# Kernel optimization log

Measured on AMD Instinct MI355X. Metric: run time of the kernel, lower is better.

Reference implementation:

```python
import jax, jax.numpy as jnp
import numpy as np

H = 16          # num_heads
W = 256         # sliding window size
LN_EPS = 1e-6
ROPE_BASE = 10000.0


def layer_norm(x, g, b):
    m = jnp.mean(x, axis=-1, keepdims=True)
    v = jnp.mean((x - m) ** 2, axis=-1, keepdims=True)
    return (x - m) * jax.lax.rsqrt(v + LN_EPS) * g + b


def rope(x):
    # x: [B, S, H, hd]; rotate-half RoPE
    S, hd = x.shape[1], x.shape[-1]
    inv_freq = 1.0 / (ROPE_BASE ** (jnp.arange(0, hd, 2, dtype=jnp.float32) / hd))
    ang = jnp.arange(S, dtype=jnp.float32)[:, None] * inv_freq[None, :]  # [S, hd/2]
    cos = jnp.concatenate([jnp.cos(ang), jnp.cos(ang)], axis=-1)[None, :, None, :]
    sin = jnp.concatenate([jnp.sin(ang), jnp.sin(ang)], axis=-1)[None, :, None, :]
    x1, x2 = jnp.split(x, 2, axis=-1)
    rot = jnp.concatenate([-x2, x1], axis=-1)
    return x * cos + rot * sin


def setup_inputs() -> dict:
    key = jax.random.key(0)
    ks = jax.random.split(key, 12)
    B, S, D, I = 2, 2048, 1024, 4096
    s = 0.02
    return {
        "hidden_states": jax.random.normal(ks[0], (B, S, D), jnp.float32),
        "wq": jax.random.normal(ks[1], (D, D), jnp.float32) * s,
        "wk": jax.random.normal(ks[2], (D, D), jnp.float32) * s,
        "wv": jax.random.normal(ks[3], (D, D), jnp.float32) * s,
        "wo": jax.random.normal(ks[4], (D, D), jnp.float32) * s,
        "w1": jax.random.normal(ks[5], (D, I), jnp.float32) * s,
        "w2": jax.random.normal(ks[6], (I, D), jnp.float32) * s,
        "w3": jax.random.normal(ks[7], (D, I), jnp.float32) * s,
        "ln1_g": jnp.ones((D,), jnp.float32),
        "ln1_b": jnp.zeros((D,), jnp.float32),
        "ln2_g": jnp.ones((D,), jnp.float32),
        "ln2_b": jnp.zeros((D,), jnp.float32),
    }


def reference(hidden_states, wq, wk, wv, wo, w1, w2, w3, ln1_g, ln1_b, ln2_g, ln2_b):
    B, S, D = hidden_states.shape
    hd = D // H

    # --- attention sub-block ---
    residual = hidden_states
    x = layer_norm(hidden_states, ln1_g, ln1_b)
    q = (x @ wq).reshape(B, S, H, hd)
    k = (x @ wk).reshape(B, S, H, hd)
    v = (x @ wv).reshape(B, S, H, hd)
    q, k = rope(q), rope(k)

    scores = jnp.einsum("bqhd,bkhd->bhqk", q, k) / jnp.sqrt(jnp.float32(hd))
    idx = jnp.arange(S)
    rel = idx[:, None] - idx[None, :]          # i - j
    mask = (rel >= 0) & (rel < W)              # causal sliding window
    scores = jnp.where(mask[None, None], scores, jnp.float32(-1e9))
    attn = jax.nn.softmax(scores, axis=-1)
    ctx = jnp.einsum("bhqk,bkhd->bqhd", attn, v).reshape(B, S, D)
    hidden_states = residual + ctx @ wo

    # --- SwiGLU MLP sub-block ---
    residual = hidden_states
    x = layer_norm(hidden_states, ln2_g, ln2_b)
    mlp = (jax.nn.silu(x @ w1) * (x @ w3)) @ w2
    return residual + mlp
```

## Files before the change

kernel.cpp:

```cpp
#include <hip/hip_runtime.h>
#include <hip/hip_bf16.h>

typedef __bf16 bf16_t;
typedef __bf16 bf16x4 __attribute__((ext_vector_type(4)));
typedef __bf16 bf16x8 __attribute__((ext_vector_type(8)));
typedef float f32x4 __attribute__((ext_vector_type(4)));

#define LN_EPS 1e-6f

__device__ __forceinline__ void gl2lds16(const void* g, void* l) {
    __builtin_amdgcn_global_load_lds(
        (const __attribute__((address_space(1))) void*)g,
        (__attribute__((address_space(3))) void*)l, 16, 0, 0);
}

__device__ __forceinline__ void block_sync() {
    __asm__ __volatile__("" ::: "memory");
    __builtin_amdgcn_s_barrier();
    __asm__ __volatile__("" ::: "memory");
}

__global__ void prep_weights_kernel(const float* __restrict__ wq, const float* __restrict__ wk,
                                    const float* __restrict__ wv, const float* __restrict__ wo,
                                    const float* __restrict__ w1, const float* __restrict__ w3,
                                    const float* __restrict__ w2, bf16_t* __restrict__ wq_t,
                                    bf16_t* __restrict__ wk_t, bf16_t* __restrict__ wv_t,
                                    bf16_t* __restrict__ wo_t, bf16_t* __restrict__ w13_t,
                                    bf16_t* __restrict__ w2_t) {
    __shared__ float tile[32][33];
    int id = blockIdx.x;
    const float* src;
    bf16_t* dst;
    int R, C, mode = 0;
    if (id < 4096) {
        int w = id >> 10;
        id &= 1023;
        src = (w == 0) ? wq : (w == 1) ? wk : (w == 2) ? wv : wo;
        dst = (w == 0) ? wq_t : (w == 1) ? wk_t : (w == 2) ? wv_t : wo_t;
        R = 1024; C = 1024;
    } else if (id < 8192) {
        id -= 4096; src = w1; dst = w13_t; R = 1024; C = 4096; mode = 1;
    } else if (id < 12288) {
        id -= 8192; src = w3; dst = w13_t; R = 1024; C = 4096; mode = 2;
    } else {
        id -= 12288; src = w2; dst = w2_t; R = 4096; C = 1024;
    }
    int tpc = C >> 5;
    int bx = id % tpc, by = id / tpc;
    int r0 = by * 32, c0 = bx * 32;
    int tx = threadIdx.x & 31;
    int ty = threadIdx.x >> 5;
#pragma unroll
    for (int i = 0; i < 4; i++) {
        int r = ty + i * 8;
        tile[r][tx] = src[(size_t)(r0 + r) * C + (c0 + tx)];
    }
    __syncthreads();
#pragma unroll
    for (int i = 0; i < 4; i++) {
        int r = ty + i * 8;
        int rr = c0 + r;
        if (mode) rr = ((rr >> 7) << 8) + (rr & 127) + ((mode == 2) ? 128 : 0);
        dst[(size_t)rr * R + (r0 + tx)] = (bf16_t)tile[tx][r];
    }
}

__global__ void ln_kernel(const float* __restrict__ x, const float* __restrict__ g,
                          const float* __restrict__ bb, bf16_t* __restrict__ out, int D) {
    int row = blockIdx.x;
    int t = threadIdx.x;
    const float4* xr = reinterpret_cast<const float4*>(x + (size_t)row * D);
    float4 v = xr[t];
    float s = v.x + v.y + v.z + v.w;
    __shared__ float sbuf[4];
    __shared__ float sbuf2[4];
    int wave = t >> 6, lane = t & 63;
#pragma unroll
    for (int o = 32; o > 0; o >>= 1) s += __shfl_xor(s, o);
    if (lane == 0) sbuf[wave] = s;
    __syncthreads();
    float mean = (sbuf[0] + sbuf[1] + sbuf[2] + sbuf[3]) / (float)D;
    float d0 = v.x - mean, d1 = v.y - mean, d2 = v.z - mean, d3 = v.w - mean;
    float sq = d0 * d0 + d1 * d1 + d2 * d2 + d3 * d3;
#pragma unroll
    for (int o = 32; o > 0; o >>= 1) sq += __shfl_xor(sq, o);
    if (lane == 0) sbuf2[wave] = sq;
    __syncthreads();
    float var = (sbuf2[0] + sbuf2[1] + sbuf2[2] + sbuf2[3]) / (float)D;
    float inv = rsqrtf(var + LN_EPS);
    float4 gv = reinterpret_cast<const float4*>(g)[t];
    float4 bv = reinterpret_cast<const float4*>(bb)[t];
    bf16_t* o0 = out + (size_t)row * D + t * 4;
    o0[0] = (bf16_t)(d0 * inv * gv.x + bv.x);
    o0[1] = (bf16_t)(d1 * inv * gv.y + bv.y);
    o0[2] = (bf16_t)(d2 * inv * gv.z + bv.z);
    o0[3] = (bf16_t)(d3 * inv * gv.w + bv.w);
}

#define G4_BK 64

template <int EPI>
__launch_bounds__(256, 2) __global__
void gemm4_kernel(const bf16_t* __restrict__ A, const bf16_t* __restrict__ Bt,
                  float* __restrict__ Cf, const float* __restrict__ aux,
                  const bf16_t* __restrict__ auxb, bf16_t* __restrict__ Cb,
                  int M, int N, int K, int lda, int ldb) {
    __shared__ __align__(16) bf16_t As[128 * G4_BK];
    __shared__ __align__(16) bf16_t Bs[128 * G4_BK];
    const int t = threadIdx.x;
    const int wave = t >> 6, lane = t & 63;
    const int lr = lane & 15, quad = lane >> 4;
    const int wm = (wave >> 1) * 64, wn = (wave & 1) * 64;

    const int gx = gridDim.x, gy = gridDim.y;
    const int nwg = gx * gy;
    const int lin = blockIdx.y * gx + blockIdx.x;
    const int qch = nwg >> 3;
    const int sw = (lin & 7) * qch + (lin >> 3);
    const int m0 = (sw / gy) * 128;
    const int n0 = (sw % gy) * 128;
    const int koff = blockIdx.z * K;

    const int srow = t >> 3;
    const int sslot = (t & 7) ^ (srow & 7);
    const bf16_t* agp = A + (size_t)(m0 + srow) * lda + koff + sslot * 8;
    const bf16_t* bgp = Bt + (size_t)(n0 + srow) * ldb + koff + sslot * 8;
    bf16_t* asl = As + t * 8;
    bf16_t* bsl = Bs + t * 8;

    int aoff[4][2], boff[4][2];
#pragma unroll
    for (int f = 0; f < 4; f++)
#pragma unroll
        for (int s = 0; s < 2; s++) {
            int ra = wm + f * 16 + lr;
            int rb = wn + f * 16 + lr;
            aoff[f][s] = ra * G4_BK + (((s * 4 + quad) ^ (ra & 7)) << 3);
            boff[f][s] = rb * G4_BK + (((s * 4 + quad) ^ (rb & 7)) << 3);
        }

    f32x4 acc[4][4];
#pragma unroll
    for (int mi = 0; mi < 4; mi++)
#pragma unroll
        for (int ni = 0; ni < 4; ni++) acc[mi][ni] = 0.f;

    for (int k0 = 0; k0 < K; k0 += G4_BK) {
#pragma unroll
        for (int i = 0; i < 4; i++)
            gl2lds16(agp + k0 + (size_t)(32 * i) * lda, asl + i * 2048);
#pragma unroll
        for (int i = 0; i < 4; i++)
            gl2lds16(bgp + k0 + (size_t)(32 * i) * ldb, bsl + i * 2048);
        __syncthreads();
#pragma unroll
        for (int s = 0; s < 2; s++) {
            bf16x8 af[4], bfv[4];
#pragma unroll
            for (int mi = 0; mi < 4; mi++)
                af[mi] = *reinterpret_cast<const bf16x8*>(&As[aoff[mi][s]]);
#pragma unroll
            for (int ni = 0; ni < 4; ni++)
                bfv[ni] = *reinterpret_cast<const bf16x8*>(&Bs[boff[ni][s]]);
#pragma unroll
            for (int mi = 0; mi < 4; mi++)
#pragma unroll
                for (int ni = 0; ni < 4; ni++)
                    acc[mi][ni] = __builtin_amdgcn_mfma_f32_16x16x32_bf16(af[mi], bfv[ni],
                                                                          acc[mi][ni], 0, 0, 0);
        }
        __syncthreads();
    }

#pragma unroll
    for (int mi = 0; mi < 4; mi++)
#pragma unroll
        for (int ni = 0; ni < 4; ni++)
#pragma unroll
            for (int j = 0; j < 4; j++) {
                int gm = m0 + wm + mi * 16 + quad * 4 + j;
                int gn = n0 + wn + ni * 16 + lr;
                size_t idx = (size_t)gm * N + gn;
                float val = acc[mi][ni][j];
                if constexpr (EPI == 1) {
                    Cf[idx] = val + aux[idx];
                }
            }
}


__device__ __forceinline__ void stage_half(const bf16_t* g, int ld, bf16_t* l,
                                           int wave, int lane) {
#pragma unroll
    for (int i = 0; i < 2; i++) {
        int lidx = (wave * 2 + i) * 64 + lane;
        int row = lidx >> 3;
        int ss = (lidx & 7) ^ (row & 7);
        gl2lds16(g + (size_t)row * ld + ss * 8, l + (wave * 2 + i) * 512);
    }
}

template <int QM, int QN>
__device__ __forceinline__ void quad_mfma(f32x4 (&acc)[2][2][4][2], const bf16x8 (&af)[4][2],
                                          const bf16x8 (&bf)[2][2]) {
#pragma unroll
    for (int fr = 0; fr < 4; fr++)
#pragma unroll
        for (int fc = 0; fc < 2; fc++)
#pragma unroll
            for (int ks = 0; ks < 2; ks++)
                acc[QM][QN][fr][fc] = __builtin_amdgcn_mfma_f32_16x16x32_bf16(
                    af[fr][ks], bf[fc][ks], acc[QM][QN][fr][fc], 0, 0, 0);
}

template <int EPI>
__launch_bounds__(512, 2) __global__
void gemm5_kernel(const bf16_t* __restrict__ A, const bf16_t* __restrict__ Bt,
                  const bf16_t* __restrict__ auxb, bf16_t* __restrict__ Cb,
                  bf16_t* __restrict__ Cb2, int M, int N, int K, int lda, int ldb) {
    extern __shared__ __align__(16) bf16_t smem[];
    bf16_t* smA = smem;
    bf16_t* smB = smem + 32768;
    const int t = threadIdx.x;
    const int wave = t >> 6, lane = t & 63;
    const int lr = lane & 15, quad = lane >> 4;
    const int rowgrp = wave >> 2;
    const int colgrp = wave & 3;
    const int cg1 = colgrp & 1, cg2 = colgrp >> 1;

    const int gx = gridDim.x, gy = gridDim.y;
    const int nwg = gx * gy;
    const int lin = blockIdx.y * gx + blockIdx.x;
    const int qch = nwg >> 3;
    const int sw = (lin & 7) * qch + (lin >> 3);
    const int m0 = (sw / gy) * 256;
    const int n0 = (sw % gy) * 256;
    const int koff = blockIdx.z * K;

    const bf16_t* Ag = A + (size_t)m0 * lda + koff;
    const bf16_t* Bg = Bt + (size_t)n0 * ldb + koff;

    int aoff[4][2], boff[2][2];
#pragma unroll
    for (int fr = 0; fr < 4; fr++)
#pragma unroll
        for (int ks = 0; ks < 2; ks++) {
            int ra = rowgrp * 64 + fr * 16 + lr;
            aoff[fr][ks] = ra * 64 + (((ks * 4 + quad) ^ (ra & 7)) << 3);
        }
#pragma unroll
    for (int fc = 0; fc < 2; fc++)
#pragma unroll
        for (int ks = 0; ks < 2; ks++) {
            int rb = cg1 * 64 + cg2 * 16 + fc * 32 + lr;
            boff[fc][ks] = rb * 64 + (((ks * 4 + quad) ^ (rb & 7)) << 3);
        }

    f32x4 acc[2][2][4][2];
#pragma unroll
    for (int qm = 0; qm < 2; qm++)
#pragma unroll
        for (int qn = 0; qn < 2; qn++)
#pragma unroll
            for (int fr = 0; fr < 4; fr++)
#pragma unroll
                for (int fc = 0; fc < 2; fc++) acc[qm][qn][fr][fc] = 0.f;

    stage_half(Ag, lda, smA, wave, lane);
    stage_half(Bg, ldb, smB, wave, lane);
    stage_half(Bg + (size_t)128 * ldb, ldb, smB + 8192, wave, lane);
    stage_half(Ag + (size_t)128 * lda, lda, smA + 8192, wave, lane);
    __asm__ __volatile__("s_waitcnt vmcnt(4)" ::: "memory");
    block_sync();

    const int NT = K >> 6;
    bf16x8 af[4][2], bf0[2][2], bf1[2][2];

    for (int tt = 0; tt < NT; ++tt) {
        const int cur = tt & 1, nxt = cur ^ 1;
        const bf16_t* A0b = smA + cur * 16384;
        const bf16_t* A1b = A0b + 8192;
        const bf16_t* B0b = smB + cur * 16384;
        const bf16_t* B1b = B0b + 8192;
        bf16_t* sA0n = smA + nxt * 16384;
        bf16_t* sB0n = smB + nxt * 16384;
        const bool pf = (tt + 1 < NT);
        const size_t kn = (size_t)(tt + 1) << 6;

#pragma unroll
        for (int fr = 0; fr < 4; fr++)
#pragma unroll
            for (int ks = 0; ks < 2; ks++)
                af[fr][ks] = *reinterpret_cast<const bf16x8*>(A0b + aoff[fr][ks]);
#pragma unroll
        for (int fc = 0; fc < 2; fc++)
#pragma unroll
            for (int ks = 0; ks < 2; ks++)
                bf0[fc][ks] = *reinterpret_cast<const bf16x8*>(B0b + boff[fc][ks]);
        if (pf) {
            stage_half(Ag + kn, lda, sA0n, wave, lane);
            stage_half(Bg + kn, ldb, sB0n, wave, lane);
        }
        block_sync();
        __asm__ __volatile__("s_waitcnt lgkmcnt(0)" ::: "memory");
        __builtin_amdgcn_sched_barrier(0);
        __builtin_amdgcn_s_setprio(1);
        quad_mfma<0, 0>(acc, af, bf0);
        __builtin_amdgcn_s_setprio(0);
        __asm__ __volatile__("s_waitcnt vmcnt(6)" ::: "memory");
        block_sync();

#pragma unroll
        for (int fc = 0; fc < 2; fc++)
#pragma unroll
            for (int ks = 0; ks < 2; ks++)
                bf1[fc][ks] = *reinterpret_cast<const bf16x8*>(B1b + boff[fc][ks]);
        if (pf) stage_half(Bg + (size_t)128 * ldb + kn, ldb, sB0n + 8192, wave, lane);
        block_sync();
        __asm__ __volatile__("s_waitcnt lgkmcnt(0)" ::: "memory");
        __builtin_amdgcn_sched_barrier(0);
        __builtin_amdgcn_s_setprio(1);
        quad_mfma<0, 1>(acc, af, bf1);
        __builtin_amdgcn_s_setprio(0);
        __asm__ __volatile__("s_waitcnt vmcnt(6)" ::: "memory");
        block_sync();

#pragma unroll
        for (int fr = 0; fr < 4; fr++)
#pragma unroll
            for (int ks = 0; ks < 2; ks++)
                af[fr][ks] = *reinterpret_cast<const bf16x8*>(A1b + aoff[fr][ks]);
        if (pf) stage_half(Ag + (size_t)128 * lda + kn, lda, sA0n + 8192, wave, lane);
        block_sync();
        __asm__ __volatile__("s_waitcnt lgkmcnt(0)" ::: "memory");
        __builtin_amdgcn_sched_barrier(0);
        __builtin_amdgcn_s_setprio(1);
        quad_mfma<1, 1>(acc, af, bf1);
        quad_mfma<1, 0>(acc, af, bf0);
        __builtin_amdgcn_s_setprio(0);
        __asm__ __volatile__("s_waitcnt vmcnt(4)" ::: "memory");
        block_sync();
    }

    if constexpr (EPI == 3) {
        if (n0 < 2048) {
            const float kfreq = -0.41524101186f;
            const int d = cg2 * 16 + lr;
            const float freq = exp2f((float)d * kfreq);
#pragma unroll
            for (int qm = 0; qm < 2; qm++)
#pragma unroll
                for (int qn = 0; qn < 2; qn++) {
                    const int gnb = n0 + qn * 128 + cg1 * 64;
#pragma unroll
                    for (int fr = 0; fr < 4; fr++)
#pragma unroll
                        for (int j = 0; j < 4; j++) {
                            int gm = m0 + qm * 128 + rowgrp * 64 + fr * 16 + quad * 4 + j;
                            float pos = (float)(gm & 2047);
                            float ang = pos * freq;
                            float sn, cs;
                            __sincosf(ang, &sn, &cs);
                            float x1 = acc[qm][qn][fr][0][j];
                            float x2 = acc[qm][qn][fr][1][j];
                            size_t idx = (size_t)gm * N + gnb + d;
                            Cb[idx] = (bf16_t)(x1 * cs - x2 * sn);
                            Cb[idx + 32] = (bf16_t)(x2 * cs + x1 * sn);
                        }
                }
        } else {
#pragma unroll
            for (int qm = 0; qm < 2; qm++)
#pragma unroll
                for (int qn = 0; qn < 2; qn++)
#pragma unroll
                    for (int fr = 0; fr < 4; fr++)
#pragma unroll
                        for (int fc = 0; fc < 2; fc++) {
                            int gmb = m0 + qm * 128 + rowgrp * 64 + fr * 16 + quad * 4;
                            int vcol = (n0 - 2048) + qn * 128 + cg1 * 64 + cg2 * 16 + fc * 32 + lr;
                            int hh = vcol >> 6, dd = vcol & 63;
                            int bb2 = gmb >> 11, ss = gmb & 2047;
                            bf16x4 pk;
#pragma unroll
                            for (int j = 0; j < 4; j++) pk[j] = (bf16_t)acc[qm][qn][fr][fc][j];
                            *reinterpret_cast<bf16x4*>(
                                &Cb2[(((size_t)(bb2 * 16 + hh)) * 64 + dd) * 2048 + ss]) = pk;
                        }
        }
    } else if constexpr (EPI == 6) {
        const int No = N >> 1;
#pragma unroll
        for (int qm = 0; qm < 2; qm++)
#pragma unroll
            for (int fr = 0; fr < 4; fr++)
#pragma unroll
                for (int fc = 0; fc < 2; fc++)
#pragma unroll
                    for (int j = 0; j < 4; j++) {
                        int gm = m0 + qm * 128 + rowgrp * 64 + fr * 16 + quad * 4 + j;
                        int c = (n0 >> 1) + cg1 * 64 + cg2 * 16 + fc * 32 + lr;
                        float a = acc[qm][0][fr][fc][j];
                        float bv = acc[qm][1][fr][fc][j];
                        float sl = a / (1.0f + __expf(-a));
                        Cb[(size_t)gm * No + c] = (bf16_t)(sl * bv);
                    }
    } else {
        size_t outoff = (EPI == 5) ? (size_t)blockIdx.z * M * N : 0;
#pragma unroll
        for (int qm = 0; qm < 2; qm++)
#pragma unroll
            for (int qn = 0; qn < 2; qn++)
#pragma unroll
                for (int fr = 0; fr < 4; fr++)
#pragma unroll
                    for (int fc = 0; fc < 2; fc++)
#pragma unroll
                        for (int j = 0; j < 4; j++) {
                            int gm = m0 + qm * 128 + rowgrp * 64 + fr * 16 + quad * 4 + j;
                            int gn = n0 + qn * 128 + cg1 * 64 + cg2 * 16 + fc * 32 + lr;
                            size_t idx = (size_t)gm * N + gn;
                            float val = acc[qm][qn][fr][fc][j];
                            if constexpr (EPI == 5) {
                                Cb[outoff + idx] = (bf16_t)val;
                            } else {
                                Cb[idx] = (bf16_t)val;
                            }
                        }
    }
}

__global__ void reduce4_kernel(const bf16_t* __restrict__ p, const float* __restrict__ hid,
                               float* __restrict__ out, int n4) {
    int i = blockIdx.x * 256 + threadIdx.x;
    if (i >= n4) return;
    size_t i4 = (size_t)i * 4;
    float4 h = *reinterpret_cast<const float4*>(hid + i4);
    const size_t stride = (size_t)4096 * 1024;
#pragma unroll
    for (int c = 0; c < 4; c++) {
        bf16x4 a = *reinterpret_cast<const bf16x4*>(p + c * stride + i4);
        h.x += (float)a[0];
        h.y += (float)a[1];
        h.z += (float)a[2];
        h.w += (float)a[3];
    }
    *reinterpret_cast<float4*>(out + i4) = h;
}

#define PSTR 40
#define QKVS 3072
__global__ __launch_bounds__(256, 2) void attn_kernel(const bf16_t* __restrict__ qkv,
                                                      const bf16_t* __restrict__ vt,
                                                      bf16_t* __restrict__ ctx, int S) {
    __shared__ __align__(16) bf16_t Pbuf[4][16 * PSTR];
    int t = threadIdx.x;
    int wave = t >> 6, lane = t & 63;
    int col = lane & 15, quad = lane >> 4;
    int h = blockIdx.y, b = blockIdx.z;
    int q0 = blockIdx.x * 64 + wave * 16;

    const bf16_t* qrow = qkv + (size_t)(b * S + q0 + col) * QKVS + h * 64;
    bf16x8 aq0 = *reinterpret_cast<const bf16x8*>(qrow + quad * 8);
    bf16x8 aq1 = *reinterpret_cast<const bf16x8*>(qrow + 32 + quad * 8);

    int jbase = q0 - 256;
    f32x4 sc[17];
#pragma unroll
    for (int kt = 0; kt < 17; kt++) {
        int j = jbase + kt * 16 + col;
        int jc = j < 0 ? 0 : (j > S - 1 ? S - 1 : j);
        const bf16_t* krow = qkv + (size_t)(b * S + jc) * QKVS + 1024 + h * 64;
        bf16x8 bk0 = *reinterpret_cast<const bf16x8*>(krow + quad * 8);
        bf16x8 bk1 = *reinterpret_cast<const bf16x8*>(krow + 32 + quad * 8);
        f32x4 c0 = {0.f, 0.f, 0.f, 0.f};
        c0 = __builtin_amdgcn_mfma_f32_16x16x32_bf16(aq0, bk0, c0, 0, 0, 0);
        c0 = __builtin_amdgcn_mfma_f32_16x16x32_bf16(aq1, bk1, c0, 0, 0, 0);
        sc[kt] = c0;
    }
#pragma unroll
    for (int kt = 0; kt < 17; kt++) {
#pragma unroll
        for (int jj = 0; jj < 4; jj++) {
            int qq = quad * 4 + jj;
            int j = jbase + kt * 16 + col;
            int rel = (q0 + qq) - j;
            bool ok = (j >= 0) && (rel >= 0) && (rel < 256);
            sc[kt][jj] = ok ? sc[kt][jj] * 0.125f : -1e30f;
        }
    }
    float sminv[4];
#pragma unroll
    for (int jj = 0; jj < 4; jj++) {
        float m = -1e30f;
#pragma unroll
        for (int kt = 0; kt < 17; kt++) m = fmaxf(m, sc[kt][jj]);
#pragma unroll
        for (int o = 1; o < 16; o <<= 1) m = fmaxf(m, __shfl_xor(m, o));
        float s = 0.f;
#pragma unroll
        for (int kt = 0; kt < 17; kt++) {
            float p = __expf(sc[kt][jj] - m);
            sc[kt][jj] = p;
            s += p;
        }
#pragma unroll
        for (int o = 1; o < 16; o <<= 1) s += __shfl_xor(s, o);
        sminv[jj] = 1.0f / s;
    }
    f32x4 o[4];
#pragma unroll
    for (int n = 0; n < 4; n++) o[n] = 0.f;
    bf16_t* myP = Pbuf[wave];
    const bf16_t* vplane = vt + ((size_t)(b * 16 + h)) * 64 * S;
#pragma unroll
    for (int c = 0; c < 9; c++) {
#pragma unroll
        for (int half = 0; half < 2; half++) {
            int kt = 2 * c + half;
#pragma unroll
            for (int jj = 0; jj < 4; jj++) {
                int qq = quad * 4 + jj;
                bf16_t pv = (kt < 17) ? (bf16_t)(sc[kt < 17 ? kt : 0][jj] * sminv[jj])
                                      : (bf16_t)0.f;
                myP[qq * PSTR + half * 16 + col] = pv;
            }
        }
        bf16x8 ap = *reinterpret_cast<const bf16x8*>(myP + col * PSTR + quad * 8);
        int key0 = jbase + c * 32 + quad * 8;
        int kc = key0 < 0 ? 0 : (key0 > S - 8 ? S - 8 : key0);
#pragma unroll
        for (int n = 0; n < 4; n++) {
            bf16x8 bv = *reinterpret_cast<const bf16x8*>(vplane + ((size_t)(n * 16 + col)) * S + kc);
            o[n] = __builtin_amdgcn_mfma_f32_16x16x32_bf16(ap, bv, o[n], 0, 0, 0);
        }
    }
#pragma unroll
    for (int n = 0; n < 4; n++)
#pragma unroll
        for (int jj = 0; jj < 4; jj++) {
            int qq = quad * 4 + jj;
            ctx[((size_t)(b * S + q0 + qq) * 16 + h) * 64 + n * 16 + col] = (bf16_t)o[n][jj];
        }
}

extern "C" void kernel_launch(void* const* d_in, const int* in_sizes, int n_in,
                              void* d_out, int out_size, void* d_ws, size_t ws_size,
                              hipStream_t stream) {
    const float* hs   = (const float*)d_in[0];
    const float* wq   = (const float*)d_in[1];
    const float* wk   = (const float*)d_in[2];
    const float* wv   = (const float*)d_in[3];
    const float* wo   = (const float*)d_in[4];
    const float* w1   = (const float*)d_in[5];
    const float* w2   = (const float*)d_in[6];
    const float* w3   = (const float*)d_in[7];
    const float* ln1g = (const float*)d_in[8];
    const float* ln1b = (const float*)d_in[9];
    const float* ln2g = (const float*)d_in[10];
    const float* ln2b = (const float*)d_in[11];
    float* out = (float*)d_out;

    const int B = 2, S = 2048, D = 1024, I = 4096;
    const int BS = B * S;

    char* ws = (char*)d_ws;
    const size_t MB = 1024 * 1024;
    bf16_t* wq_t  = (bf16_t*)(ws + 0 * MB);
    bf16_t* wk_t  = (bf16_t*)(ws + 2 * MB);
    bf16_t* wv_t  = (bf16_t*)(ws + 4 * MB);
    bf16_t* wo_t  = (bf16_t*)(ws + 6 * MB);
    bf16_t* w13_t = (bf16_t*)(ws + 8 * MB);
    bf16_t* w2_t  = (bf16_t*)(ws + 24 * MB);
    bf16_t* x_b   = (bf16_t*)(ws + 32 * MB);
    float*  hid   = (float*)(ws + 40 * MB);
    bf16_t* x2_b  = (bf16_t*)(ws + 56 * MB);
    bf16_t* qkvb  = (bf16_t*)(ws + 64 * MB);
    bf16_t* vt    = (bf16_t*)(ws + 88 * MB);
    bf16_t* ctxb  = (bf16_t*)(ws + 96 * MB);
    bf16_t* hbuf  = (bf16_t*)(ws + 96 * MB);
    bf16_t* pker  = (bf16_t*)(ws + 64 * MB);

    hipFuncSetAttribute(reinterpret_cast<const void*>(&gemm5_kernel<3>),
                        hipFuncAttributeMaxDynamicSharedMemorySize, 131072);
    hipFuncSetAttribute(reinterpret_cast<const void*>(&gemm5_kernel<5>),
                        hipFuncAttributeMaxDynamicSharedMemorySize, 131072);
    hipFuncSetAttribute(reinterpret_cast<const void*>(&gemm5_kernel<6>),
                        hipFuncAttributeMaxDynamicSharedMemorySize, 131072);

    dim3 tb(256);
    dim3 tb5(512);

    prep_weights_kernel<<<dim3(16384), tb, 0, stream>>>(wq, wk, wv, wo, w1, w3, w2, wq_t, wk_t,
                                                        wv_t, wo_t, w13_t, w2_t);

    ln_kernel<<<BS, tb, 0, stream>>>(hs, ln1g, ln1b, x_b, D);

    gemm5_kernel<3><<<dim3(BS / 256, 3072 / 256), tb5, 131072, stream>>>(
        x_b, wq_t, nullptr, qkvb, vt, BS, 3072, D, D, D);

    attn_kernel<<<dim3(S / 64, 16, B), tb, 0, stream>>>(qkvb, vt, ctxb, S);

    gemm4_kernel<1><<<dim3(BS / 128, D / 128), tb, 0, stream>>>(
        ctxb, wo_t, hid, hs, nullptr, nullptr, BS, D, D, D, D);

    ln_kernel<<<BS, tb, 0, stream>>>(hid, ln2g, ln2b, x2_b, D);

    gemm5_kernel<6><<<dim3(BS / 256, 8192 / 256), tb5, 131072, stream>>>(
        x2_b, w13_t, nullptr, hbuf, nullptr, BS, 8192, D, D, D);

    gemm5_kernel<5><<<dim3(BS / 256, D / 256, 4), tb5, 131072, stream>>>(
        hbuf, w2_t, nullptr, pker, nullptr, BS, D, 1024, I, I);
    reduce4_kernel<<<dim3(BS * D / 4 / 256), tb, 0, stream>>>(pker, hid, out, BS * D / 4);
}
```

Measured before the change: 357.7 us.

## Prefetch first A half-tile two iterations ahead in 256x256 GEMM pipeline

Restructures the global-to-LDS prefetch schedule of the 256x256 bf16 GEMM. The first A half-tile for iteration k+2 is now loaded into the current buffer once its last use finishes, partway through the final MFMA quad. Most intermediate vmcnt waits are removed in favour of one wait per iteration. This deepens load lookahead to hide global latency. It adds an extra barrier mid-iteration and depends on the vmcnt accounting being correct for every buffer reuse.

```diff
diff --git a/kernel.cpp b/kernel.cpp
--- a/kernel.cpp
+++ b/kernel.cpp
@@ -215,7 +215,7 @@
 
 template <int EPI>
 __launch_bounds__(512, 2) __global__
-void gemm5_kernel(const bf16_t* __restrict__ A, const bf16_t* __restrict__ Bt,
+void gemm6_kernel(const bf16_t* __restrict__ A, const bf16_t* __restrict__ Bt,
                   const bf16_t* __restrict__ auxb, bf16_t* __restrict__ Cb,
                   bf16_t* __restrict__ Cb2, int M, int N, int K, int lda, int ldb) {
     extern __shared__ __align__(16) bf16_t smem[];
@@ -266,14 +266,20 @@
 #pragma unroll
                 for (int fc = 0; fc < 2; fc++) acc[qm][qn][fr][fc] = 0.f;
 
+    const int NT = K >> 6;
+
     stage_half(Ag, lda, smA, wave, lane);
     stage_half(Bg, ldb, smB, wave, lane);
     stage_half(Bg + (size_t)128 * ldb, ldb, smB + 8192, wave, lane);
     stage_half(Ag + (size_t)128 * lda, lda, smA + 8192, wave, lane);
-    __asm__ __volatile__("s_waitcnt vmcnt(4)" ::: "memory");
+    if (NT > 1) {
+        stage_half(Ag + 64, lda, smA + 16384, wave, lane);
+        __asm__ __volatile__("s_waitcnt vmcnt(2)" ::: "memory");
+    } else {
+        __asm__ __volatile__("s_waitcnt vmcnt(0)" ::: "memory");
+    }
     block_sync();
 
-    const int NT = K >> 6;
     bf16x8 af[4][2], bf0[2][2], bf1[2][2];
 
     for (int tt = 0; tt < NT; ++tt) {
@@ -282,10 +288,13 @@
         const bf16_t* A1b = A0b + 8192;
         const bf16_t* B0b = smB + cur * 16384;
         const bf16_t* B1b = B0b + 8192;
-        bf16_t* sA0n = smA + nxt * 16384;
-        bf16_t* sB0n = smB + nxt * 16384;
-        const bool pf = (tt + 1 < NT);
-        const size_t kn = (size_t)(tt + 1) << 6;
+        bf16_t* sAn = smA + nxt * 16384;
+        bf16_t* sBn = smB + nxt * 16384;
+        bf16_t* sAc = smA + cur * 16384;
+        const bool pf1 = (tt + 1 < NT);
+        const bool pf2 = (tt + 2 < NT);
+        const size_t kn1 = (size_t)(tt + 1) << 6;
+        const size_t kn2 = (size_t)(tt + 2) << 6;
 
 #pragma unroll
         for (int fr = 0; fr < 4; fr++)
@@ -297,17 +306,13 @@
 #pragma unroll
             for (int ks = 0; ks < 2; ks++)
                 bf0[fc][ks] = *reinterpret_cast<const bf16x8*>(B0b + boff[fc][ks]);
-        if (pf) {
-            stage_half(Ag + kn, lda, sA0n, wave, lane);
-            stage_half(Bg + kn, ldb, sB0n, wave, lane);
-        }
+        if (pf1) stage_half(Bg + kn1, ldb, sBn, wave, lane);
         block_sync();
         __asm__ __volatile__("s_waitcnt lgkmcnt(0)" ::: "memory");
         __builtin_amdgcn_sched_barrier(0);
         __builtin_amdgcn_s_setprio(1);
         quad_mfma<0, 0>(acc, af, bf0);
         __builtin_amdgcn_s_setprio(0);
-        __asm__ __volatile__("s_waitcnt vmcnt(6)" ::: "memory");
         block_sync();
 
 #pragma unroll
@@ -315,14 +320,13 @@
 #pragma unroll
             for (int ks = 0; ks < 2; ks++)
                 bf1[fc][ks] = *reinterpret_cast<const bf16x8*>(B1b + boff[fc][ks]);
-        if (pf) stage_half(Bg + (size_t)128 * ldb + kn, ldb, sB0n + 8192, wave, lane);
+        if (pf1) stage_half(Bg + (size_t)128 * ldb + kn1, ldb, sBn + 8192, wave, lane);
         block_sync();
         __asm__ __volatile__("s_waitcnt lgkmcnt(0)" ::: "memory");
         __builtin_amdgcn_sched_barrier(0);
         __builtin_amdgcn_s_setprio(1);
         quad_mfma<0, 1>(acc, af, bf1);
         __builtin_amdgcn_s_setprio(0);
-        __asm__ __volatile__("s_waitcnt vmcnt(6)" ::: "memory");
         block_sync();
 
 #pragma unroll
@@ -330,15 +334,20 @@
 #pragma unroll
             for (int ks = 0; ks < 2; ks++)
                 af[fr][ks] = *reinterpret_cast<const bf16x8*>(A1b + aoff[fr][ks]);
-        if (pf) stage_half(Ag + (size_t)128 * lda + kn, lda, sA0n + 8192, wave, lane);
+        if (pf1) stage_half(Ag + (size_t)128 * lda + kn1, lda, sAn + 8192, wave, lane);
         block_sync();
         __asm__ __volatile__("s_waitcnt lgkmcnt(0)" ::: "memory");
         __builtin_amdgcn_sched_barrier(0);
         __builtin_amdgcn_s_setprio(1);
         quad_mfma<1, 1>(acc, af, bf1);
+        __builtin_amdgcn_s_setprio(0);
+        block_sync();
+
+        if (pf2) stage_half(Ag + kn2, lda, sAc, wave, lane);
+        __builtin_amdgcn_s_setprio(1);
         quad_mfma<1, 0>(acc, af, bf0);
         __builtin_amdgcn_s_setprio(0);
-        __asm__ __volatile__("s_waitcnt vmcnt(4)" ::: "memory");
+        __asm__ __volatile__("s_waitcnt vmcnt(2)" ::: "memory");
         block_sync();
     }
 
@@ -581,22 +590,22 @@
     bf16_t* hbuf  = (bf16_t*)(ws + 96 * MB);
     bf16_t* pker  = (bf16_t*)(ws + 64 * MB);
 
-    hipFuncSetAttribute(reinterpret_cast<const void*>(&gemm5_kernel<3>),
+    hipFuncSetAttribute(reinterpret_cast<const void*>(&gemm6_kernel<3>),
                         hipFuncAttributeMaxDynamicSharedMemorySize, 131072);
-    hipFuncSetAttribute(reinterpret_cast<const void*>(&gemm5_kernel<5>),
+    hipFuncSetAttribute(reinterpret_cast<const void*>(&gemm6_kernel<5>),
                         hipFuncAttributeMaxDynamicSharedMemorySize, 131072);
-    hipFuncSetAttribute(reinterpret_cast<const void*>(&gemm5_kernel<6>),
+    hipFuncSetAttribute(reinterpret_cast<const void*>(&gemm6_kernel<6>),
                         hipFuncAttributeMaxDynamicSharedMemorySize, 131072);
 
     dim3 tb(256);
-    dim3 tb5(512);
+    dim3 tb6(512);
 
     prep_weights_kernel<<<dim3(16384), tb, 0, stream>>>(wq, wk, wv, wo, w1, w3, w2, wq_t, wk_t,
                                                         wv_t, wo_t, w13_t, w2_t);
 
     ln_kernel<<<BS, tb, 0, stream>>>(hs, ln1g, ln1b, x_b, D);
 
-    gemm5_kernel<3><<<dim3(BS / 256, 3072 / 256), tb5, 131072, stream>>>(
+    gemm6_kernel<3><<<dim3(BS / 256, 3072 / 256), tb6, 131072, stream>>>(
         x_b, wq_t, nullptr, qkvb, vt, BS, 3072, D, D, D);
 
     attn_kernel<<<dim3(S / 64, 16, B), tb, 0, stream>>>(qkvb, vt, ctxb, S);
@@ -606,10 +615,10 @@
 
     ln_kernel<<<BS, tb, 0, stream>>>(hid, ln2g, ln2b, x2_b, D);
 
-    gemm5_kernel<6><<<dim3(BS / 256, 8192 / 256), tb5, 131072, stream>>>(
+    gemm6_kernel<6><<<dim3(BS / 256, 8192 / 256), tb6, 131072, stream>>>(
         x2_b, w13_t, nullptr, hbuf, nullptr, BS, 8192, D, D, D);
 
-    gemm5_kernel<5><<<dim3(BS / 256, D / 256, 4), tb5, 131072, stream>>>(
+    gemm6_kernel<5><<<dim3(BS / 256, D / 256, 4), tb6, 131072, stream>>>(
         hbuf, w2_t, nullptr, pker, nullptr, BS, D, 1024, I, I);
     reduce4_kernel<<<dim3(BS * D / 4 / 256), tb, 0, stream>>>(pker, hid, out, BS * D / 4);
 }
```

Measured after the change: 356.0 us. No clear change (-0.5%).
